# Optimization experiments

Hardware: AMD Instinct MI355X
Metric: run time of the kernel (lower is better)

Reference implementation:

```python
import jax, jax.numpy as jnp
import numpy as np


def _gcn_conv(x, edge_index, W, b):
    """Faithful PyG GCNConv: add self-loops, symmetric norm, scatter-sum, bias."""
    n = x.shape[0]
    loop = jnp.arange(n, dtype=edge_index.dtype)
    src = jnp.concatenate([edge_index[0], loop])  # [E+n]
    dst = jnp.concatenate([edge_index[1], loop])
    # in-degree at dst (edge_weight = 1), as in gcn_norm
    deg = jax.ops.segment_sum(jnp.ones(src.shape[0], x.dtype), dst, num_segments=n)
    dinv = jnp.where(deg > 0, jax.lax.rsqrt(deg), 0.0)
    norm = dinv[src] * dinv[dst]                  # [E+n]
    h = x @ W                                     # [n, C] small GEMM
    msg = h[src] * norm[:, None]                  # gather + scale (dominant traffic)
    out = jax.ops.segment_sum(msg, dst, num_segments=n)  # scatter-sum
    return out + b


def setup_inputs() -> dict:
    key = jax.random.key(0)
    ks = jax.random.split(key, 8)
    N, E, C = 50000, 1000000, 64
    scale = 1.0 / np.sqrt(C)
    return {
        "x_star": jax.random.normal(ks[0], (N, C), jnp.float32),
        "x_gal": jax.random.normal(ks[1], (N, C), jnp.float32),
        "edge_ss_near": jax.random.randint(ks[2], (2, E), 0, N, jnp.int64),
        "edge_ss_far": jax.random.randint(ks[3], (2, E), 0, N, jnp.int64),
        "edge_gg_near": jax.random.randint(ks[4], (2, E), 0, N, jnp.int64),
        "W_ss_near": jax.random.normal(ks[5], (C, C), jnp.float32) * scale,
        "W_ss_far": jax.random.normal(ks[6], (C, C), jnp.float32) * scale,
        "W_gg_near": jax.random.normal(ks[7], (C, C), jnp.float32) * scale,
        "b_ss_near": jnp.zeros((C,), jnp.float32),
        "b_ss_far": jnp.zeros((C,), jnp.float32),
        "b_gg_near": jnp.zeros((C,), jnp.float32),
    }


def reference(x_star, x_gal, edge_ss_near, edge_ss_far, edge_gg_near,
              W_ss_near, W_ss_far, W_gg_near,
              b_ss_near, b_ss_far, b_gg_near):
    # HeteroConv with aggr='sum': per-edge-type GCNConv, summed per dst node type.
    out_star = (_gcn_conv(x_star, edge_ss_near, W_ss_near, b_ss_near)
                + _gcn_conv(x_star, edge_ss_far, W_ss_far, b_ss_far))
    out_gal = _gcn_conv(x_gal, edge_gg_near, W_gg_near, b_gg_near)
    return out_star, out_gal
```

## Files before the change

### kernel.cpp

```cpp
#include <hip/hip_runtime.h>
#include <hip/hip_fp16.h>

#define CCH 64
#define BKT 256
#define NBMAX 200
#define CAP 6144
#define PCH 8192
#define GR 64

typedef int int4a __attribute__((ext_vector_type(4), aligned(4)));

__device__ __forceinline__ int scan256ex(int v, int t, int* wsum) {
    int s = v;
    #pragma unroll
    for (int off = 1; off < 64; off <<= 1) {
        int u = __shfl_up(s, off, 64);
        if ((t & 63) >= off) s += u;
    }
    if ((t & 63) == 63) wsum[t >> 6] = s;
    __syncthreads();
    int wpre = 0;
    #pragma unroll
    for (int j = 0; j < 4; ++j) if (j < (t >> 6)) wpre += wsum[j];
    return wpre + s - v;
}

__global__ void __launch_bounds__(256) k_part(const int* __restrict__ e0,
        const int* __restrict__ e1, const int* __restrict__ e2,
        int* __restrict__ bucketcur, unsigned* __restrict__ bdata,
        int E, int NB) {
    int c = blockIdx.y;
    const int* ed = (c == 0) ? e0 : (c == 1) ? e1 : e2;
    int base = blockIdx.x * PCH;
    int nE = E - base; if (nE > PCH) nE = PCH;
    __shared__ unsigned staged[PCH];
    __shared__ int hist[NBMAX];
    __shared__ int off[NBMAX];
    __shared__ int wsum[4];
    int t = threadIdx.x;
    if (t < NB) hist[t] = 0;
    __syncthreads();
    const int* dd = ed + E;
    for (int k = t * 4; k < nE; k += 1024) {
        if (k + 3 < nE) {
            int4a d = *(const int4a*)(dd + base + k);
            atomicAdd(&hist[d.x >> 8], 1); atomicAdd(&hist[d.y >> 8], 1);
            atomicAdd(&hist[d.z >> 8], 1); atomicAdd(&hist[d.w >> 8], 1);
        } else {
            for (int j = k; j < nE; ++j) atomicAdd(&hist[dd[base + j] >> 8], 1);
        }
    }
    __syncthreads();
    int v = (t < NB) ? hist[t] : 0;
    int lbase = scan256ex(v, t, wsum);
    if (t < NB) {
        int old = atomicAdd(&bucketcur[c * NB + t], v);
        off[t] = t * CAP + old - lbase;
    }
    __syncthreads();
    if (t < NB) hist[t] = lbase;
    __syncthreads();
    for (int k = t * 4; k < nE; k += 1024) {
        if (k + 3 < nE) {
            int4a s4 = *(const int4a*)(ed + base + k);
            int4a d4 = *(const int4a*)(ed + E + base + k);
            int sl;
            sl = atomicAdd(&hist[d4.x >> 8], 1); staged[sl] = (unsigned)s4.x | ((unsigned)d4.x << 16);
            sl = atomicAdd(&hist[d4.y >> 8], 1); staged[sl] = (unsigned)s4.y | ((unsigned)d4.y << 16);
            sl = atomicAdd(&hist[d4.z >> 8], 1); staged[sl] = (unsigned)s4.z | ((unsigned)d4.z << 16);
            sl = atomicAdd(&hist[d4.w >> 8], 1); staged[sl] = (unsigned)s4.w | ((unsigned)d4.w << 16);
        } else {
            for (int j = k; j < nE; ++j) {
                int s0 = ed[base + j];
                int d0 = ed[E + base + j];
                int sl = atomicAdd(&hist[d0 >> 8], 1);
                staged[sl] = (unsigned)s0 | ((unsigned)d0 << 16);
            }
        }
    }
    __syncthreads();
    unsigned* bo = bdata + (size_t)c * NB * CAP;
    for (int sI = t; sI < nE; sI += 256) {
        unsigned rec = staged[sI];
        int b = (int)(rec >> 24);
        bo[off[b] + sI] = rec;
    }
}

__global__ void __launch_bounds__(256) k_sort(const unsigned* __restrict__ bdata,
        const int* __restrict__ bucketcur, int* __restrict__ sdat,
        int* __restrict__ rst, int* __restrict__ ren, float* __restrict__ dinv,
        __half* __restrict__ zrow, int N, int NB) {
    int c = blockIdx.y, b = blockIdx.x;
    __shared__ unsigned staged[CAP];
    __shared__ unsigned sorted[CAP];
    __shared__ int cnt[BKT];
    __shared__ int cur[BKT];
    __shared__ int wsum[4];
    int t = threadIdx.x;
    if (c == 0 && b == 0 && t < 32) ((float*)zrow)[t] = 0.f;
    cnt[t] = 0;
    __syncthreads();
    int n = bucketcur[c * NB + b]; if (n > CAP) n = CAP;
    size_t g0 = (size_t)c * NB * CAP + (size_t)b * CAP;
    for (int i = t; i < n; i += 256) staged[i] = bdata[g0 + i];
    __syncthreads();
    for (int i = t; i < n; i += 256)
        atomicAdd(&cnt[(staged[i] >> 16) & 255], 1);
    __syncthreads();
    int v = cnt[t];
    int ex = scan256ex(v, t, wsum);
    cur[t] = ex;
    int row = b * BKT + t;
    if (row < N) {
        rst[c * N + row] = b * CAP + ex;
        ren[c * N + row] = b * CAP + ex + v;
        dinv[(size_t)c * N + row] = rsqrtf((float)(v + 1));
    }
    __syncthreads();
    for (int i = t; i < n; i += 256) {
        unsigned r = staged[i];
        int slot = atomicAdd(&cur[(r >> 16) & 255], 1);
        sorted[slot] = r & 0xFFFFu;
    }
    __syncthreads();
    int* so = sdat + (size_t)c * NB * CAP;
    for (int i = t; i < n; i += 256) so[(size_t)b * CAP + i] = (int)sorted[i];
}

__global__ void __launch_bounds__(256) k_gemm_all(const float* __restrict__ xs_,
        const float* __restrict__ xg_, const float* __restrict__ W0,
        const float* __restrict__ W1, const float* __restrict__ W2,
        const float* __restrict__ dinv, __half* __restrict__ h16, int N) {
    int star = (blockIdx.y == 0);
    const float* x = star ? xs_ : xg_;
    __shared__ float Ws[2][CCH * CCH];
    __shared__ float xT[CCH * (GR + 1)];
    int t = threadIdx.x;
    int row0 = blockIdx.x * GR;
    size_t NC = (size_t)N * CCH;
    if (star) {
        #pragma unroll
        for (int j = 0; j < 4; ++j) {
            int idx = j * 1024 + t * 4;
            *(float4*)(&Ws[0][idx]) = *(const float4*)(W0 + idx);
            *(float4*)(&Ws[1][idx]) = *(const float4*)(W1 + idx);
        }
    } else {
        #pragma unroll
        for (int j = 0; j < 4; ++j) {
            int idx = j * 1024 + t * 4;
            *(float4*)(&Ws[0][idx]) = *(const float4*)(W2 + idx);
        }
    }
    #pragma unroll
    for (int j = 0; j < 4; ++j) {
        int idx = t + j * 256;
        int r = idx >> 4;
        int c0 = (idx & 15) * 4;
        int row = row0 + r;
        float4 v = make_float4(0.f, 0.f, 0.f, 0.f);
        if (row < N) v = *(const float4*)(x + (size_t)row * CCH + c0);
        xT[(c0 + 0) * (GR + 1) + r] = v.x;
        xT[(c0 + 1) * (GR + 1) + r] = v.y;
        xT[(c0 + 2) * (GR + 1) + r] = v.z;
        xT[(c0 + 3) * (GR + 1) + r] = v.w;
    }
    __syncthreads();
    int c4 = (t & 15) * 4;
    int r0 = (t >> 4) * 4;
    if (star) {
        float4 a0 = make_float4(0.f, 0.f, 0.f, 0.f), a1 = a0, a2 = a0, a3 = a0;
        float4 d0 = a0, d1 = a0, d2 = a0, d3 = a0;
        #pragma unroll 4
        for (int k = 0; k < CCH; ++k) {
            float4 wv = *(float4*)(&Ws[0][k * CCH + c4]);
            float4 uv = *(float4*)(&Ws[1][k * CCH + c4]);
            float x0 = xT[k * (GR + 1) + r0 + 0];
            float x1 = xT[k * (GR + 1) + r0 + 1];
            float x2 = xT[k * (GR + 1) + r0 + 2];
            float x3 = xT[k * (GR + 1) + r0 + 3];
            a0.x += x0 * wv.x; a0.y += x0 * wv.y; a0.z += x0 * wv.z; a0.w += x0 * wv.w;
            a1.x += x1 * wv.x; a1.y += x1 * wv.y; a1.z += x1 * wv.z; a1.w += x1 * wv.w;
            a2.x += x2 * wv.x; a2.y += x2 * wv.y; a2.z += x2 * wv.z; a2.w += x2 * wv.w;
            a3.x += x3 * wv.x; a3.y += x3 * wv.y; a3.z += x3 * wv.z; a3.w += x3 * wv.w;
            d0.x += x0 * uv.x; d0.y += x0 * uv.y; d0.z += x0 * uv.z; d0.w += x0 * uv.w;
            d1.x += x1 * uv.x; d1.y += x1 * uv.y; d1.z += x1 * uv.z; d1.w += x1 * uv.w;
            d2.x += x2 * uv.x; d2.y += x2 * uv.y; d2.z += x2 * uv.z; d2.w += x2 * uv.w;
            d3.x += x3 * uv.x; d3.y += x3 * uv.y; d3.z += x3 * uv.z; d3.w += x3 * uv.w;
        }
        float4 av[4] = {a0, a1, a2, a3};
        float4 dv4[4] = {d0, d1, d2, d3};
        #pragma unroll
        for (int i = 0; i < 4; ++i) {
            int row = row0 + r0 + i;
            if (row < N) {
                float dd0 = dinv[row];
                float dd1 = dinv[N + row];
                union { __half2 h2[2]; float2 f2; } u;
                u.h2[0] = __floats2half2_rn(av[i].x * dd0, av[i].y * dd0);
                u.h2[1] = __floats2half2_rn(av[i].z * dd0, av[i].w * dd0);
                *(float2*)(h16 + (size_t)row * CCH + c4) = u.f2;
                u.h2[0] = __floats2half2_rn(dv4[i].x * dd1, dv4[i].y * dd1);
                u.h2[1] = __floats2half2_rn(dv4[i].z * dd1, dv4[i].w * dd1);
                *(float2*)(h16 + NC + (size_t)row * CCH + c4) = u.f2;
            }
        }
    } else {
        float4 a0 = make_float4(0.f, 0.f, 0.f, 0.f), a1 = a0, a2 = a0, a3 = a0;
        #pragma unroll 8
        for (int k = 0; k < CCH; ++k) {
            float4 wv = *(float4*)(&Ws[0][k * CCH + c4]);
            float x0 = xT[k * (GR + 1) + r0 + 0];
            float x1 = xT[k * (GR + 1) + r0 + 1];
            float x2 = xT[k * (GR + 1) + r0 + 2];
            float x3 = xT[k * (GR + 1) + r0 + 3];
            a0.x += x0 * wv.x; a0.y += x0 * wv.y; a0.z += x0 * wv.z; a0.w += x0 * wv.w;
            a1.x += x1 * wv.x; a1.y += x1 * wv.y; a1.z += x1 * wv.z; a1.w += x1 * wv.w;
            a2.x += x2 * wv.x; a2.y += x2 * wv.y; a2.z += x2 * wv.z; a2.w += x2 * wv.w;
            a3.x += x3 * wv.x; a3.y += x3 * wv.y; a3.z += x3 * wv.z; a3.w += x3 * wv.w;
        }
        float4 av[4] = {a0, a1, a2, a3};
        #pragma unroll
        for (int i = 0; i < 4; ++i) {
            int row = row0 + r0 + i;
            if (row < N) {
                float dd = dinv[2 * N + row];
                union { __half2 h2[2]; float2 f2; } u;
                u.h2[0] = __floats2half2_rn(av[i].x * dd, av[i].y * dd);
                u.h2[1] = __floats2half2_rn(av[i].z * dd, av[i].w * dd);
                *(float2*)(h16 + 2 * NC + (size_t)row * CCH + c4) = u.f2;
            }
        }
    }
}

__device__ __forceinline__ float4 gat4p(const __half* __restrict__ p, int l16) {
    union { float2 f2; __half2 h2[2]; } u;
    u.f2 = ((const float2*)p)[l16];
    float2 a = __half22float2(u.h2[0]);
    float2 b = __half22float2(u.h2[1]);
    return make_float4(a.x, a.y, b.x, b.y);
}

__device__ __forceinline__ void acc4(float4& a, float4 v) {
    a.x += v.x; a.y += v.y; a.z += v.z; a.w += v.w;
}

__global__ void __launch_bounds__(256) k_pull(const int* __restrict__ rst,
        const int* __restrict__ ren,
        const int* __restrict__ sdat, const __half* __restrict__ h16,
        const float* __restrict__ dinv, const __half* __restrict__ zrow,
        const float* __restrict__ b0, const float* __restrict__ b1,
        const float* __restrict__ b2,
        float* __restrict__ out, int N, int GAPE) {
    int row = blockIdx.x * 4 + (threadIdx.x >> 6);
    if (row >= 2 * N) return;
    int lane = threadIdx.x & 63;
    int q = lane >> 4;
    int l16 = lane & 15;
    size_t NC = (size_t)N * CCH;

    const __half* hcL;
    const int* sdL;
    int beg, end;
    float ddL;
    float4 bias;
    float* op;
    float4 acc = make_float4(0.f, 0.f, 0.f, 0.f);
    if (row < N) {
        int cv = q >> 1;
        int bg = rst[cv * N + row], eg = ren[cv * N + row];
        int mid = (bg + eg) >> 1;
        beg = (q & 1) ? mid : bg;
        end = (q & 1) ? eg : mid;
        hcL = h16 + (size_t)cv * NC;
        sdL = sdat + (size_t)cv * GAPE;
        ddL = dinv[cv * N + row];
        if (!(q & 1)) acc = gat4p(hcL + (size_t)row * CCH, l16);
        float4 bv0 = ((const float4*)b0)[l16];
        float4 bv1 = ((const float4*)b1)[l16];
        bias = make_float4(bv0.x + bv1.x, bv0.y + bv1.y,
                           bv0.z + bv1.z, bv0.w + bv1.w);
        op = out + (size_t)row * CCH;
    } else {
        int r = row - N;
        int bg = rst[2 * N + r], eg = ren[2 * N + r];
        int len = eg - bg;
        beg = bg + ((len * q) >> 2);
        end = bg + ((len * (q + 1)) >> 2);
        hcL = h16 + 2 * NC;
        sdL = sdat + 2 * (size_t)GAPE;
        ddL = dinv[2 * N + r];
        if (q == 0) acc = gat4p(hcL + (size_t)r * CCH, l16);
        bias = ((const float4*)b2)[l16];
        op = out + NC + (size_t)r * CCH;
    }

    int i = beg;
    for (; i + 7 < end; i += 8) {
        int4a q0 = *(const int4a*)(sdL + i);
        int4a q1 = *(const int4a*)(sdL + i + 4);
        float4 v0 = gat4p(hcL + (size_t)q0.x * CCH, l16);
        float4 v1 = gat4p(hcL + (size_t)q0.y * CCH, l16);
        float4 v2 = gat4p(hcL + (size_t)q0.z * CCH, l16);
        float4 v3 = gat4p(hcL + (size_t)q0.w * CCH, l16);
        float4 v4 = gat4p(hcL + (size_t)q1.x * CCH, l16);
        float4 v5 = gat4p(hcL + (size_t)q1.y * CCH, l16);
        float4 v6 = gat4p(hcL + (size_t)q1.z * CCH, l16);
        float4 v7 = gat4p(hcL + (size_t)q1.w * CCH, l16);
        acc4(acc, v0); acc4(acc, v1); acc4(acc, v2); acc4(acc, v3);
        acc4(acc, v4); acc4(acc, v5); acc4(acc, v6); acc4(acc, v7);
    }
    if (i < end) {
        int4a q0 = *(const int4a*)(sdL + i);
        int4a q1 = *(const int4a*)(sdL + i + 4);
        const __half* p0 = hcL + (size_t)q0.x * CCH;
        const __half* p1 = (i + 1 < end) ? hcL + (size_t)q0.y * CCH : zrow;
        const __half* p2 = (i + 2 < end) ? hcL + (size_t)q0.z * CCH : zrow;
        const __half* p3 = (i + 3 < end) ? hcL + (size_t)q0.w * CCH : zrow;
        const __half* p4 = (i + 4 < end) ? hcL + (size_t)q1.x * CCH : zrow;
        const __half* p5 = (i + 5 < end) ? hcL + (size_t)q1.y * CCH : zrow;
        const __half* p6 = (i + 6 < end) ? hcL + (size_t)q1.z * CCH : zrow;
        const __half* p7 = (i + 7 < end) ? hcL + (size_t)q1.w * CCH : zrow;
        float4 v0 = gat4p(p0, l16);
        float4 v1 = gat4p(p1, l16);
        float4 v2 = gat4p(p2, l16);
        float4 v3 = gat4p(p3, l16);
        float4 v4 = gat4p(p4, l16);
        float4 v5 = gat4p(p5, l16);
        float4 v6 = gat4p(p6, l16);
        float4 v7 = gat4p(p7, l16);
        acc4(acc, v0); acc4(acc, v1); acc4(acc, v2); acc4(acc, v3);
        acc4(acc, v4); acc4(acc, v5); acc4(acc, v6); acc4(acc, v7);
    }

    float4 t;
    t.x = acc.x * ddL; t.y = acc.y * ddL; t.z = acc.z * ddL; t.w = acc.w * ddL;
    t.x += __shfl_xor(t.x, 16, 64); t.y += __shfl_xor(t.y, 16, 64);
    t.z += __shfl_xor(t.z, 16, 64); t.w += __shfl_xor(t.w, 16, 64);
    t.x += __shfl_xor(t.x, 32, 64); t.y += __shfl_xor(t.y, 32, 64);
    t.z += __shfl_xor(t.z, 32, 64); t.w += __shfl_xor(t.w, 32, 64);
    if (lane < 16) {
        t.x += bias.x; t.y += bias.y; t.z += bias.z; t.w += bias.w;
        ((float4*)op)[l16] = t;
    }
}

static inline size_t align256(size_t x) { return (x + 255) & ~(size_t)255; }

extern "C" void kernel_launch(void* const* d_in, const int* in_sizes, int n_in,
                              void* d_out, int out_size, void* d_ws, size_t ws_size,
                              hipStream_t stream) {
    const float* x_star = (const float*)d_in[0];
    const float* x_gal  = (const float*)d_in[1];
    const int*   e_ssn  = (const int*)d_in[2];
    const int*   e_ssf  = (const int*)d_in[3];
    const int*   e_ggn  = (const int*)d_in[4];
    const float* W_ssn  = (const float*)d_in[5];
    const float* W_ssf  = (const float*)d_in[6];
    const float* W_ggn  = (const float*)d_in[7];
    const float* b_ssn  = (const float*)d_in[8];
    const float* b_ssf  = (const float*)d_in[9];
    const float* b_ggn  = (const float*)d_in[10];

    const int N  = in_sizes[0] / CCH;
    const int E  = in_sizes[2] / 2;
    const size_t NC = (size_t)N * CCH;
    const int NB   = (N + BKT - 1) / BKT;
    const int NBLK = (E + PCH - 1) / PCH;
    const int GAPE = NB * CAP;

    char* w = (char*)d_ws;
    __half*   h16    = (__half*)w;   w += align256((size_t)3 * NC * 2);
    float*    dinv   = (float*)w;    w += align256((size_t)3 * N * 4);
    unsigned* bdata  = (unsigned*)w; w += align256((size_t)3 * GAPE * 4);
    int*      sdat   = (int*)w;      w += align256((size_t)3 * GAPE * 4);
    int*      bucketcur = (int*)w;   w += align256((size_t)3 * NB * 4);
    int*      rst    = (int*)w;      w += align256((size_t)3 * N * 4);
    int*      ren    = (int*)w;      w += align256((size_t)3 * N * 4);
    __half*   zrow   = (__half*)w;   w += align256((size_t)CCH * 2);

    const int B = 256;

    hipMemsetAsync(bucketcur, 0, (size_t)3 * NB * 4, stream);
    k_part<<<dim3(NBLK, 3), B, 0, stream>>>(e_ssn, e_ssf, e_ggn,
                                            bucketcur, bdata, E, NB);
    k_sort<<<dim3(NB, 3), B, 0, stream>>>(bdata, bucketcur, sdat,
                                          rst, ren, dinv, zrow, N, NB);
    k_gemm_all<<<dim3((N + GR - 1) / GR, 2), B, 0, stream>>>(x_star, x_gal,
                                                             W_ssn, W_ssf, W_ggn,
                                                             dinv, h16, N);
    k_pull<<<(2 * N + 3) / 4, B, 0, stream>>>(rst, ren, sdat, h16, dinv, zrow,
                                              b_ssn, b_ssf, b_ggn,
                                              (float*)d_out, N, GAPE);
}
```

Before: 205.1 us.

## Pad per-row edge lists to multiples of 8 with a zero sentinel row

The sort kernel now pads each destination row's neighbour list to a multiple of 8 entries, filled with index N. Each h16 slab gets an extra zero row at index N, so the pull kernel can drop its masked tail iteration and run only full 8-wide gather loops. The pull launch is also split into two launches, one for star rows and one for galaxy rows. The trade-off is extra gather traffic on padding entries (up to 7 per row per conv), a larger sdat buffer, and a second kernel launch.

```diff
diff --git a/kernel.cpp b/kernel.cpp
--- a/kernel.cpp
+++ b/kernel.cpp
@@ -5,6 +5,7 @@
 #define BKT 256
 #define NBMAX 200
 #define CAP 6144
+#define SCAP 6912
 #define PCH 8192
 #define GR 64
 
@@ -90,15 +91,15 @@
 __global__ void __launch_bounds__(256) k_sort(const unsigned* __restrict__ bdata,
         const int* __restrict__ bucketcur, int* __restrict__ sdat,
         int* __restrict__ rst, int* __restrict__ ren, float* __restrict__ dinv,
-        __half* __restrict__ zrow, int N, int NB) {
+        int N, int NB) {
     int c = blockIdx.y, b = blockIdx.x;
     __shared__ unsigned staged[CAP];
-    __shared__ unsigned sorted[CAP];
+    __shared__ unsigned sorted[SCAP];
     __shared__ int cnt[BKT];
     __shared__ int cur[BKT];
     __shared__ int wsum[4];
+    __shared__ int sh_tot;
     int t = threadIdx.x;
-    if (c == 0 && b == 0 && t < 32) ((float*)zrow)[t] = 0.f;
     cnt[t] = 0;
     __syncthreads();
     int n = bucketcur[c * NB + b]; if (n > CAP) n = CAP;
@@ -109,14 +110,19 @@
         atomicAdd(&cnt[(staged[i] >> 16) & 255], 1);
     __syncthreads();
     int v = cnt[t];
-    int ex = scan256ex(v, t, wsum);
-    cur[t] = ex;
+    int pl = (v + 7) & ~7;
+    int pex = scan256ex(pl, t, wsum);
+    cur[t] = pex;
     int row = b * BKT + t;
     if (row < N) {
-        rst[c * N + row] = b * CAP + ex;
-        ren[c * N + row] = b * CAP + ex + v;
+        rst[c * N + row] = b * SCAP + pex;
+        ren[c * N + row] = b * SCAP + pex + pl;
         dinv[(size_t)c * N + row] = rsqrtf((float)(v + 1));
     }
+    if (t == 255) sh_tot = pex + pl;
+    __syncthreads();
+    int ptot = sh_tot;
+    for (int i = t; i < ptot; i += 256) sorted[i] = (unsigned)N;
     __syncthreads();
     for (int i = t; i < n; i += 256) {
         unsigned r = staged[i];
@@ -124,8 +130,8 @@
         sorted[slot] = r & 0xFFFFu;
     }
     __syncthreads();
-    int* so = sdat + (size_t)c * NB * CAP;
-    for (int i = t; i < n; i += 256) so[(size_t)b * CAP + i] = (int)sorted[i];
+    int* so = sdat + (size_t)c * NB * SCAP + (size_t)b * SCAP;
+    for (int i = t; i < ptot; i += 256) so[i] = (int)sorted[i];
 }
 
 __global__ void __launch_bounds__(256) k_gemm_all(const float* __restrict__ xs_,
@@ -138,7 +144,15 @@
     __shared__ float xT[CCH * (GR + 1)];
     int t = threadIdx.x;
     int row0 = blockIdx.x * GR;
-    size_t NC = (size_t)N * CCH;
+    size_t NC = (size_t)(N + 1) * CCH;
+    if (blockIdx.x == 0) {
+        if (star) {
+            if (t < 32) ((float*)(h16 + (size_t)N * CCH))[t] = 0.f;
+            else if (t < 64) ((float*)(h16 + NC + (size_t)N * CCH))[t - 32] = 0.f;
+        } else {
+            if (t < 32) ((float*)(h16 + 2 * NC + (size_t)N * CCH))[t] = 0.f;
+        }
+    }
     if (star) {
         #pragma unroll
         for (int j = 0; j < 4; ++j) {
@@ -250,16 +264,17 @@
 __global__ void __launch_bounds__(256) k_pull(const int* __restrict__ rst,
         const int* __restrict__ ren,
         const int* __restrict__ sdat, const __half* __restrict__ h16,
-        const float* __restrict__ dinv, const __half* __restrict__ zrow,
+        const float* __restrict__ dinv,
         const float* __restrict__ b0, const float* __restrict__ b1,
         const float* __restrict__ b2,
-        float* __restrict__ out, int N, int GAPE) {
-    int row = blockIdx.x * 4 + (threadIdx.x >> 6);
+        float* __restrict__ out, int N, int GAPE, int row0) {
+    int row = row0 + blockIdx.x * 4 + (threadIdx.x >> 6);
     if (row >= 2 * N) return;
     int lane = threadIdx.x & 63;
     int q = lane >> 4;
     int l16 = lane & 15;
-    size_t NC = (size_t)N * CCH;
+    size_t NC = (size_t)(N + 1) * CCH;
+    size_t NOUT = (size_t)N * CCH;
 
     const __half* hcL;
     const int* sdL;
@@ -271,9 +286,10 @@
     if (row < N) {
         int cv = q >> 1;
         int bg = rst[cv * N + row], eg = ren[cv * N + row];
-        int mid = (bg + eg) >> 1;
-        beg = (q & 1) ? mid : bg;
-        end = (q & 1) ? eg : mid;
+        int nb = (eg - bg) >> 3;
+        int h1 = (nb + 1) >> 1;
+        beg = (q & 1) ? bg + 8 * h1 : bg;
+        end = (q & 1) ? eg : bg + 8 * h1;
         hcL = h16 + (size_t)cv * NC;
         sdL = sdat + (size_t)cv * GAPE;
         ddL = dinv[cv * N + row];
@@ -286,19 +302,18 @@
     } else {
         int r = row - N;
         int bg = rst[2 * N + r], eg = ren[2 * N + r];
-        int len = eg - bg;
-        beg = bg + ((len * q) >> 2);
-        end = bg + ((len * (q + 1)) >> 2);
+        int nb = (eg - bg) >> 3;
+        beg = bg + 8 * ((nb * q) >> 2);
+        end = bg + 8 * ((nb * (q + 1)) >> 2);
         hcL = h16 + 2 * NC;
         sdL = sdat + 2 * (size_t)GAPE;
         ddL = dinv[2 * N + r];
         if (q == 0) acc = gat4p(hcL + (size_t)r * CCH, l16);
         bias = ((const float4*)b2)[l16];
-        op = out + NC + (size_t)r * CCH;
-    }
-
-    int i = beg;
-    for (; i + 7 < end; i += 8) {
+        op = out + NOUT + (size_t)r * CCH;
+    }
+
+    for (int i = beg; i < end; i += 8) {
         int4a q0 = *(const int4a*)(sdL + i);
         int4a q1 = *(const int4a*)(sdL + i + 4);
         float4 v0 = gat4p(hcL + (size_t)q0.x * CCH, l16);
@@ -309,28 +324,6 @@
         float4 v5 = gat4p(hcL + (size_t)q1.y * CCH, l16);
         float4 v6 = gat4p(hcL + (size_t)q1.z * CCH, l16);
         float4 v7 = gat4p(hcL + (size_t)q1.w * CCH, l16);
-        acc4(acc, v0); acc4(acc, v1); acc4(acc, v2); acc4(acc, v3);
-        acc4(acc, v4); acc4(acc, v5); acc4(acc, v6); acc4(acc, v7);
-    }
-    if (i < end) {
-        int4a q0 = *(const int4a*)(sdL + i);
-        int4a q1 = *(const int4a*)(sdL + i + 4);
-        const __half* p0 = hcL + (size_t)q0.x * CCH;
-        const __half* p1 = (i + 1 < end) ? hcL + (size_t)q0.y * CCH : zrow;
-        const __half* p2 = (i + 2 < end) ? hcL + (size_t)q0.z * CCH : zrow;
-        const __half* p3 = (i + 3 < end) ? hcL + (size_t)q0.w * CCH : zrow;
-        const __half* p4 = (i + 4 < end) ? hcL + (size_t)q1.x * CCH : zrow;
-        const __half* p5 = (i + 5 < end) ? hcL + (size_t)q1.y * CCH : zrow;
-        const __half* p6 = (i + 6 < end) ? hcL + (size_t)q1.z * CCH : zrow;
-        const __half* p7 = (i + 7 < end) ? hcL + (size_t)q1.w * CCH : zrow;
-        float4 v0 = gat4p(p0, l16);
-        float4 v1 = gat4p(p1, l16);
-        float4 v2 = gat4p(p2, l16);
-        float4 v3 = gat4p(p3, l16);
-        float4 v4 = gat4p(p4, l16);
-        float4 v5 = gat4p(p5, l16);
-        float4 v6 = gat4p(p6, l16);
-        float4 v7 = gat4p(p7, l16);
         acc4(acc, v0); acc4(acc, v1); acc4(acc, v2); acc4(acc, v3);
         acc4(acc, v4); acc4(acc, v5); acc4(acc, v6); acc4(acc, v7);
     }
@@ -366,20 +359,19 @@
 
     const int N  = in_sizes[0] / CCH;
     const int E  = in_sizes[2] / 2;
-    const size_t NC = (size_t)N * CCH;
+    const size_t NC1 = (size_t)(N + 1) * CCH;
     const int NB   = (N + BKT - 1) / BKT;
     const int NBLK = (E + PCH - 1) / PCH;
-    const int GAPE = NB * CAP;
+    const int GAPE = NB * SCAP;
 
     char* w = (char*)d_ws;
-    __half*   h16    = (__half*)w;   w += align256((size_t)3 * NC * 2);
+    __half*   h16    = (__half*)w;   w += align256((size_t)3 * NC1 * 2);
     float*    dinv   = (float*)w;    w += align256((size_t)3 * N * 4);
-    unsigned* bdata  = (unsigned*)w; w += align256((size_t)3 * GAPE * 4);
+    unsigned* bdata  = (unsigned*)w; w += align256((size_t)3 * NB * CAP * 4);
     int*      sdat   = (int*)w;      w += align256((size_t)3 * GAPE * 4);
     int*      bucketcur = (int*)w;   w += align256((size_t)3 * NB * 4);
     int*      rst    = (int*)w;      w += align256((size_t)3 * N * 4);
     int*      ren    = (int*)w;      w += align256((size_t)3 * N * 4);
-    __half*   zrow   = (__half*)w;   w += align256((size_t)CCH * 2);
 
     const int B = 256;
 
@@ -387,11 +379,14 @@
     k_part<<<dim3(NBLK, 3), B, 0, stream>>>(e_ssn, e_ssf, e_ggn,
                                             bucketcur, bdata, E, NB);
     k_sort<<<dim3(NB, 3), B, 0, stream>>>(bdata, bucketcur, sdat,
-                                          rst, ren, dinv, zrow, N, NB);
+                                          rst, ren, dinv, N, NB);
     k_gemm_all<<<dim3((N + GR - 1) / GR, 2), B, 0, stream>>>(x_star, x_gal,
                                                              W_ssn, W_ssf, W_ggn,
                                                              dinv, h16, N);
-    k_pull<<<(2 * N + 3) / 4, B, 0, stream>>>(rst, ren, sdat, h16, dinv, zrow,
-                                              b_ssn, b_ssf, b_ggn,
-                                              (float*)d_out, N, GAPE);
-}
+    k_pull<<<(N + 3) / 4, B, 0, stream>>>(rst, ren, sdat, h16, dinv,
+                                          b_ssn, b_ssf, b_ggn,
+                                          (float*)d_out, N, GAPE, 0);
+    k_pull<<<(N + 3) / 4, B, 0, stream>>>(rst, ren, sdat, h16, dinv,
+                                          b_ssn, b_ssf, b_ggn,
+                                          (float*)d_out, N, GAPE, N);
+}
```

New measurement: 217.9 us. 1.06x slower.
